# Kernel optimization log

Hardware: AMD Instinct MI355X
Metric: run time of the kernel (lower is better)

## Reference

```python
import jax, jax.numpy as jnp
import numpy as np

NEG_SLOPE = 0.2

def _gat_layer(x, src, dst, W, a_src, a_dst, bias, concat):
    # x: [N, F_in]; W: [F_in, H*C]; a_src/a_dst: [H, C]; bias: [H*C] or [C]
    N = x.shape[0]
    H, C = a_src.shape
    h = (x @ W).reshape(N, H, C)                      # node features per head
    e_src = jnp.einsum('nhc,hc->nh', h, a_src)        # [N, H]
    e_dst = jnp.einsum('nhc,hc->nh', h, a_dst)        # [N, H]
    e = jax.nn.leaky_relu(e_src[src] + e_dst[dst], NEG_SLOPE)  # [E, H]
    # segment softmax over incoming edges of each destination node
    m = jax.ops.segment_max(e, dst, num_segments=N)   # [N, H]
    p = jnp.exp(e - m[dst])
    denom = jax.ops.segment_sum(p, dst, num_segments=N)
    alpha = p / denom[dst]                            # [E, H]
    msg = h[src] * alpha[:, :, None]                  # [E, H, C]
    out = jax.ops.segment_sum(msg, dst, num_segments=N)  # [N, H, C]
    if concat:
        out = out.reshape(N, H * C) + bias
    else:
        out = out.mean(axis=1) + bias
    return out, alpha


def setup_inputs() -> dict:
    key = jax.random.key(0)
    ks = jax.random.split(key, 12)
    N, E = 20000, 320000
    F_in, Ch, Co, H = 256, 64, 64, 8
    x = jax.random.normal(ks[0], (N, F_in), dtype=jnp.float32)
    edge_index = jax.random.randint(ks[1], (2, E), 0, N, dtype=jnp.int64)
    s = 0.05
    return {
        'x': x,
        'edge_index': edge_index,
        'W1': jax.random.normal(ks[2], (F_in, H * Ch), dtype=jnp.float32) * s,
        'att_src1': jax.random.normal(ks[3], (H, Ch), dtype=jnp.float32) * s,
        'att_dst1': jax.random.normal(ks[4], (H, Ch), dtype=jnp.float32) * s,
        'b1': jnp.zeros((H * Ch,), dtype=jnp.float32),
        'W2': jax.random.normal(ks[5], (H * Ch, H * Co), dtype=jnp.float32) * s,
        'att_src2': jax.random.normal(ks[6], (H, Co), dtype=jnp.float32) * s,
        'att_dst2': jax.random.normal(ks[7], (H, Co), dtype=jnp.float32) * s,
        'b2': jnp.zeros((Co,), dtype=jnp.float32),
    }


def reference(x, edge_index, W1, att_src1, att_dst1, b1, W2, att_src2, att_dst2, b2):
    N = x.shape[0]
    # PyG GATConv adds self-loops by default
    loop = jnp.arange(N, dtype=edge_index.dtype)
    src = jnp.concatenate([edge_index[0], loop])
    dst = jnp.concatenate([edge_index[1], loop])
    h1, alpha1 = _gat_layer(x, src, dst, W1, att_src1, att_dst1, b1, concat=True)
    h1 = jax.nn.relu(h1)
    h2, alpha2 = _gat_layer(h1, src, dst, W2, att_src2, att_dst2, b2, concat=False)
    return h2, alpha1, alpha2
```

## Files before the change

### kernel.cpp

```cpp
#include <hip/hip_runtime.h>

#define H 8
#define C 64
#define HC 512
#define NEG 0.2f

typedef __attribute__((ext_vector_type(8))) _Float16 half8v;
typedef __attribute__((ext_vector_type(4))) _Float16 half4v;
typedef __attribute__((ext_vector_type(4))) float f32x4;

__device__ __forceinline__ float leaky(float x) { return x > 0.f ? x : NEG * x; }

#define GLOAD_LDS16(gp, lp) \
  __builtin_amdgcn_global_load_lds((const __attribute__((address_space(1))) unsigned int*)(gp), \
                                   (__attribute__((address_space(3))) unsigned int*)(lp), 16, 0, 0)

__global__ void k_degree(const int* __restrict__ ei, int E, int N, int* __restrict__ deg) {
    int e = blockIdx.x * blockDim.x + threadIdx.x;
    int Et = E + N;
    if (e >= Et) return;
    int d = (e < E) ? ei[E + e] : (e - E);
    atomicAdd(&deg[d], 1);
}

__global__ __launch_bounds__(1024) void k_scan(const int* __restrict__ deg, int N, int* __restrict__ row_start) {
    __shared__ int part[1024];
    int t = threadIdx.x;
    int chunk = (N + 1023) >> 10;
    int lo = t * chunk, hi = min(lo + chunk, N);
    int s = 0;
    for (int i = lo; i < hi; ++i) s += deg[i];
    part[t] = s;
    __syncthreads();
    for (int off = 1; off < 1024; off <<= 1) {
        int v = (t >= off) ? part[t - off] : 0;
        __syncthreads();
        part[t] += v;
        __syncthreads();
    }
    int base = (t == 0) ? 0 : part[t - 1];
    for (int i = lo; i < hi; ++i) { row_start[i] = base; base += deg[i]; }
    if (t == 1023) row_start[N] = part[1023];
}

__global__ void k_fill(const int* __restrict__ ei, int E, int N,
                       const int* __restrict__ row_start, int* __restrict__ cursor,
                       int* __restrict__ csr_src, int* __restrict__ csr_eid,
                       int* __restrict__ csr_dst) {
    int e = blockIdx.x * blockDim.x + threadIdx.x;
    int Et = E + N;
    if (e >= Et) return;
    int d, s;
    if (e < E) { s = ei[e]; d = ei[E + e]; } else { s = e - E; d = s; }
    int pos = atomicAdd(&cursor[d], 1);
    int idx = row_start[d] + pos;
    csr_src[idx] = s;
    csr_eid[idx] = e;
    csr_dst[idx] = d;
}

__global__ void k_tofp16(const float* __restrict__ in, _Float16* __restrict__ out, int n4) {
    int i = blockIdx.x * blockDim.x + threadIdx.x;
    if (i >= n4) return;
    float4 v = reinterpret_cast<const float4*>(in)[i];
    half4v h;
    h[0] = (_Float16)v.x; h[1] = (_Float16)v.y;
    h[2] = (_Float16)v.z; h[3] = (_Float16)v.w;
    reinterpret_cast<half4v*>(out)[i] = h;
}

__global__ void k_tcast(const float* __restrict__ W, _Float16* __restrict__ th, int K, int Nc) {
    int idx = blockIdx.x * blockDim.x + threadIdx.x;
    if (idx >= K * Nc) return;
    int c = idx / K, k = idx - c * K;
    th[idx] = (_Float16)W[(long)k * Nc + c];
}

__global__ __launch_bounds__(256) void k_gemm_mfma(const _Float16* __restrict__ A,
                                                   const _Float16* __restrict__ B,
                                                   _Float16* __restrict__ Cc, int M, int K, int Pb, int Mpad) {
    __shared__ _Float16 lA[8192], lB[8192];
    int bid = blockIdx.x;
    int panel = ((bid >> 5) << 3) + (bid & 7);
    int colb  = (bid >> 3) & 3;
    if (panel >= Pb) return;
    int tid = threadIdx.x;
    int w = tid >> 6, lane = tid & 63;
    int wr = w >> 1, wc = w & 1;
    int r0 = panel * 128, c0 = colb * 128;
    f32x4 acc[4][4] = {};
    int frag_off = ((lane >> 4) * 16 + (lane & 15)) * 8;

    int rb0 = tid >> 6, kc0 = (tid >> 4) & 3, r16_0 = tid & 15;
    int rb1 = (256 + tid) >> 6, kc1 = ((256 + tid) >> 4) & 3;
    long gaBase0 = (long)(r0 + rb0 * 16 + r16_0) * K + kc0 * 8;
    long gbBase0 = (long)(c0 + rb0 * 16 + r16_0) * K + kc0 * 8;
    long gaBase1 = (long)(r0 + rb1 * 16 + r16_0) * K + kc1 * 8;
    long gbBase1 = (long)(c0 + rb1 * 16 + r16_0) * K + kc1 * 8;
    int ldst0 = (w * 64) * 8;
    int ldst1 = (256 + w * 64) * 8;

#define STAGE(buf, k0)  do { \
        int off = (buf) * 4096; \
        GLOAD_LDS16(A + gaBase0 + (k0), lA + off + ldst0); \
        GLOAD_LDS16(B + gbBase0 + (k0), lB + off + ldst0); \
        GLOAD_LDS16(A + gaBase1 + (k0), lA + off + ldst1); \
        GLOAD_LDS16(B + gbBase1 + (k0), lB + off + ldst1); \
    } while (0)

    int nk = K >> 5;
    STAGE(0, 0);
    __syncthreads();
    int cur = 0;
    for (int t = 0; t < nk; ++t) {
        if (t + 1 < nk) STAGE(cur ^ 1, (t + 1) * 32);
        int off = cur * 4096;
        half8v fa[4], fb[4];
        #pragma unroll
        for (int m = 0; m < 4; ++m) {
            int sa = off + (wr * 4 + m) * 512 + frag_off;
            fa[m] = *reinterpret_cast<half8v*>(&lA[sa]);
            int sb = off + (wc * 4 + m) * 512 + frag_off;
            fb[m] = *reinterpret_cast<half8v*>(&lB[sb]);
        }
        #pragma unroll
        for (int m = 0; m < 4; ++m)
            #pragma unroll
            for (int n = 0; n < 4; ++n)
                acc[m][n] = __builtin_amdgcn_mfma_f32_16x16x32_f16(fa[m], fb[n], acc[m][n], 0, 0, 0);
        __syncthreads();
        cur ^= 1;
    }
#undef STAGE

    int head = colb * 2 + wc;
    long hbase = (long)head * Mpad * 64;
    #pragma unroll
    for (int m = 0; m < 4; ++m)
        #pragma unroll
        for (int j = 0; j < 4; ++j) {
            int gr = r0 + wr * 64 + m * 16 + (lane >> 4) * 4 + j;
            if (gr < M) {
                #pragma unroll
                for (int n = 0; n < 4; ++n)
                    Cc[hbase + (long)gr * 64 + n * 16 + (lane & 15)] = (_Float16)acc[m][n][j];
            }
        }
}

__global__ __launch_bounds__(512) void k_edot(const half8v* __restrict__ hp8,
                                              const float* __restrict__ a_src,
                                              const float* __restrict__ a_dst,
                                              float* __restrict__ e_src, float* __restrict__ e_dst,
                                              int N, int Mpad) {
    int h = threadIdx.x >> 6, lane = threadIdx.x & 63;
    int n8 = lane >> 3, cg = lane & 7;
    int n = blockIdx.x * 8 + n8;
    bool valid = (n < N);
    int nc = valid ? n : (N - 1);
    float as[8], ad[8];
    #pragma unroll
    for (int k = 0; k < 8; ++k) {
        as[k] = a_src[h * 64 + cg * 8 + k];
        ad[k] = a_dst[h * 64 + cg * 8 + k];
    }
    half8v hv = hp8[(long)h * Mpad * 8 + (long)nc * 8 + cg];
    float es = 0.f, ed = 0.f;
    #pragma unroll
    for (int k = 0; k < 8; ++k) {
        es = fmaf((float)hv[k], as[k], es);
        ed = fmaf((float)hv[k], ad[k], ed);
    }
    #pragma unroll
    for (int o = 1; o <= 4; o <<= 1) {
        es += __shfl_xor(es, o);
        ed += __shfl_xor(ed, o);
    }
    if (valid && cg == 0) {
        e_src[n * 8 + h] = es;
        e_dst[n * 8 + h] = ed;
    }
}

__global__ __launch_bounds__(512) void k_edge(const float* __restrict__ e_src,
                                              const float* __restrict__ e_dst,
                                              const int* __restrict__ row_start,
                                              const int* __restrict__ csr_src,
                                              int2* __restrict__ sp,
                                              float* __restrict__ inv_nm,
                                              float* __restrict__ inv_hm,
                                              int N, int Et) {
    int wid = threadIdx.x >> 6, lane = threadIdx.x & 63;
    int g = lane >> 5;
    int eg = (lane >> 3) & 3;
    int h = lane & 7;
    int n = blockIdx.x * 16 + wid * 2 + g;
    bool valid = (n < N);
    int nc = valid ? n : (N - 1);
    int row = row_start[nc];
    int deg = row_start[nc + 1] - row;
    float ed = e_dst[nc * 8 + h];
    long hEt = (long)h * Et;
    int it = (deg + 3) >> 2;
    int itmax = max(it, __shfl_xor(it, 32));
    const int* cs = csr_src + row + eg;
    int s_nf = cs[0];
    float psum = 0.f;
    for (int c = 0; c < itmax; ++c) {
        int s = s_nf;
        if (c + 1 < itmax) s_nf = cs[(c + 1) * 4];
        int e0 = c * 4 + eg;
        float es = e_src[s * 8 + h];
        float p = (e0 < deg) ? __expf(leaky(es + ed)) : 0.f;
        psum += p;
        if (valid && e0 < deg)
            sp[hEt + row + e0] = make_int2(s, __float_as_int(p));
    }
    psum += __shfl_xor(psum, 8);
    psum += __shfl_xor(psum, 16);
    float inv = 1.0f / psum;
    if (valid && eg == 0) {
        inv_nm[n * 8 + h] = inv;
        inv_hm[h * N + n] = inv;
    }
}

__global__ void k_alpha(const int* __restrict__ csr_dst, const int* __restrict__ csr_eid,
                        const int2* __restrict__ sp, const float* __restrict__ inv_nm,
                        float* __restrict__ alpha, int Et) {
    int idx = blockIdx.x * blockDim.x + threadIdx.x;
    if (idx >= Et) return;
    int d = csr_dst[idx], eid = csr_eid[idx];
    const float4* i4 = reinterpret_cast<const float4*>(inv_nm) + (long)d * 2;
    float4 i0 = i4[0], i1 = i4[1];
    float iv[8] = {i0.x, i0.y, i0.z, i0.w, i1.x, i1.y, i1.z, i1.w};
    float r[8];
    #pragma unroll
    for (int h = 0; h < 8; ++h)
        r[h] = __int_as_float(sp[(long)h * Et + idx].y) * iv[h];
    float4* o4 = reinterpret_cast<float4*>(alpha) + (long)eid * 2;
    o4[0] = make_float4(r[0], r[1], r[2], r[3]);
    o4[1] = make_float4(r[4], r[5], r[6], r[7]);
}

__global__ __launch_bounds__(256) void k_gather(const half8v* __restrict__ hp8,
                                                const int* __restrict__ row_start,
                                                const int2* __restrict__ sp,
                                                const float* __restrict__ inv_hm,
                                                const float* __restrict__ bias,
                                                _Float16* __restrict__ h1,
                                                _Float16* __restrict__ accq,
                                                int N, int Mpad, int Et, int concat) {
    int wid = threadIdx.x >> 6, lane = threadIdx.x & 63;
    int bid = blockIdx.x;
    int h = bid & 7;
    int g = lane >> 5;
    int eg = (lane >> 3) & 3;
    int cg = lane & 7;
    int n = (bid >> 3) * 8 + wid * 2 + g;
    bool valid = (n < N);
    int nc = valid ? n : (N - 1);
    const half8v* hpb = hp8 + (long)h * Mpad * 8 + cg;
    int row = row_start[nc];
    int deg = row_start[nc + 1] - row;
    int it = (deg + 15) >> 4;
    int itmax = max(it, __shfl_xor(it, 32));
    float acc[8] = {};
    const int2* pp = sp + (long)h * Et + row + eg * 4;
    int2 q0 = pp[0], q1 = pp[1], q2 = pp[2], q3 = pp[3];
    int ebase = eg * 4;
    for (int c = 0; c < itmax; ++c) {
        int2 a0 = q0, a1 = q1, a2 = q2, a3 = q3;
        if (c + 1 < itmax) {
            pp += 16;
            q0 = pp[0]; q1 = pp[1]; q2 = pp[2]; q3 = pp[3];
        }
        int e0 = c * 16 + ebase;
        float p0 = (e0 + 0 < deg) ? __int_as_float(a0.y) : 0.f;
        float p1 = (e0 + 1 < deg) ? __int_as_float(a1.y) : 0.f;
        float p2 = (e0 + 2 < deg) ? __int_as_float(a2.y) : 0.f;
        float p3 = (e0 + 3 < deg) ? __int_as_float(a3.y) : 0.f;
        half8v h0 = hpb[(long)a0.x * 8];
        half8v h1v = hpb[(long)a1.x * 8];
        half8v h2 = hpb[(long)a2.x * 8];
        half8v h3 = hpb[(long)a3.x * 8];
        #pragma unroll
        for (int k = 0; k < 8; ++k) {
            acc[k] = fmaf((float)h0[k], p0, acc[k]);
            acc[k] = fmaf((float)h1v[k], p1, acc[k]);
            acc[k] = fmaf((float)h2[k], p2, acc[k]);
            acc[k] = fmaf((float)h3[k], p3, acc[k]);
        }
    }
    #pragma unroll
    for (int o = 8; o <= 16; o <<= 1)
        #pragma unroll
        for (int k = 0; k < 8; ++k)
            acc[k] += __shfl_xor(acc[k], o);
    if (!valid) return;
    float inv = inv_hm[h * N + n];
    if (eg == 0) {
        if (concat) {
            half8v hh;
            #pragma unroll
            for (int k = 0; k < 8; ++k) {
                float v = fmaf(acc[k], inv, bias[h * 64 + cg * 8 + k]);
                v = v > 0.f ? v : 0.f;
                hh[k] = (_Float16)v;
            }
            reinterpret_cast<half8v*>(h1)[(long)n * 64 + h * 8 + cg] = hh;
        } else {
            half8v hv2;
            #pragma unroll
            for (int k = 0; k < 8; ++k) hv2[k] = (_Float16)(acc[k] * inv);
            reinterpret_cast<half8v*>(accq)[(long)h * Mpad * 8 + (long)n * 8 + cg] = hv2;
        }
    }
}

__global__ void k_mean(const _Float16* __restrict__ accq, const float* __restrict__ bias,
                       float* __restrict__ out, int N, int Mpad) {
    int i = blockIdx.x * blockDim.x + threadIdx.x;
    if (i >= N * 8) return;
    int n = i >> 3, cg = i & 7;
    float s[8] = {};
    #pragma unroll
    for (int h = 0; h < 8; ++h) {
        half8v v = reinterpret_cast<const half8v*>(accq)[(long)h * Mpad * 8 + (long)n * 8 + cg];
        #pragma unroll
        for (int k = 0; k < 8; ++k) s[k] += (float)v[k];
    }
    float4 r0, r1;
    r0.x = s[0] * 0.125f + bias[cg * 8 + 0];
    r0.y = s[1] * 0.125f + bias[cg * 8 + 1];
    r0.z = s[2] * 0.125f + bias[cg * 8 + 2];
    r0.w = s[3] * 0.125f + bias[cg * 8 + 3];
    r1.x = s[4] * 0.125f + bias[cg * 8 + 4];
    r1.y = s[5] * 0.125f + bias[cg * 8 + 5];
    r1.z = s[6] * 0.125f + bias[cg * 8 + 6];
    r1.w = s[7] * 0.125f + bias[cg * 8 + 7];
    float4* o4 = reinterpret_cast<float4*>(out + (long)n * 64 + cg * 8);
    o4[0] = r0;
    o4[1] = r1;
}

extern "C" void kernel_launch(void* const* d_in, const int* in_sizes, int n_in,
                              void* d_out, int out_size, void* d_ws, size_t ws_size,
                              hipStream_t stream) {
    const float* x   = (const float*)d_in[0];
    const int*   ei  = (const int*)d_in[1];
    const float* W1  = (const float*)d_in[2];
    const float* as1 = (const float*)d_in[3];
    const float* ad1 = (const float*)d_in[4];
    const float* b1  = (const float*)d_in[5];
    const float* W2  = (const float*)d_in[6];
    const float* as2 = (const float*)d_in[7];
    const float* ad2 = (const float*)d_in[8];
    const float* b2  = (const float*)d_in[9];

    int N  = in_sizes[0] / 256;
    int E  = in_sizes[1] / 2;
    int Et = E + N;
    int K1 = 256;
    int Mb   = (N + 127) / 128;
    int Mpad = Mb * 128;
    const int PAD = 64;

    float* out    = (float*)d_out;
    float* h2_out = out;
    float* alpha1 = out + (size_t)N * 64;
    float* alpha2 = alpha1 + (size_t)Et * H;

    _Float16* hpre = (_Float16*)d_ws;
    _Float16* h1   = hpre + (size_t)Mpad * HC;
    _Float16* accq = h1 + (size_t)Mpad * HC;
    _Float16* xh   = accq + (size_t)Mpad * HC;
    _Float16* W1t  = xh + (size_t)Mpad * K1;
    _Float16* W2t  = W1t + (size_t)HC * K1;
    float* eS     = (float*)(W2t + (size_t)HC * HC);
    float* eD     = eS + (size_t)N * H;
    float* invnm  = eD + (size_t)N * H;
    float* invhm  = invnm + (size_t)N * H;
    int2* sp      = (int2*)(invhm + (size_t)N * H);
    int*   deg    = (int*)(sp + (size_t)H * Et + PAD);
    int*   cursor = deg + N;
    int*   row_st = cursor + N;
    int*   csr_src= row_st + N + 1;
    int*   csr_eid= csr_src + Et + PAD;
    int*   csr_dst= csr_eid + Et;

    hipMemsetAsync(deg, 0, (size_t)2 * N * sizeof(int), stream);
    hipMemsetAsync(sp + (size_t)H * Et, 0, PAD * sizeof(int2), stream);
    hipMemsetAsync(csr_src + Et, 0, PAD * sizeof(int), stream);
    int tb = 256;
    k_degree<<<(Et + tb - 1) / tb, tb, 0, stream>>>(ei, E, N, deg);
    k_scan<<<1, 1024, 0, stream>>>(deg, N, row_st);
    k_fill<<<(Et + tb - 1) / tb, tb, 0, stream>>>(ei, E, N, row_st, cursor, csr_src, csr_eid, csr_dst);

    int n4 = N * K1 / 4;
    k_tofp16<<<(n4 + tb - 1) / tb, tb, 0, stream>>>(x, xh, n4);
    k_tcast<<<(K1 * HC + tb - 1) / tb, tb, 0, stream>>>(W1, W1t, K1, HC);
    k_tcast<<<(HC * HC + tb - 1) / tb, tb, 0, stream>>>(W2, W2t, HC, HC);

    int Pb8 = ((Mb + 7) / 8) * 8;
    int ggemm = Pb8 * 4;
    int gedot = (N + 7) / 8;
    int gedge = (N + 15) / 16;
    int ggath = ((N + 7) / 8) * 8;
    k_gemm_mfma<<<ggemm, 256, 0, stream>>>(xh, W1t, hpre, N, K1, Mb, Mpad);
    k_edot<<<gedot, 512, 0, stream>>>((const half8v*)hpre, as1, ad1, eS, eD, N, Mpad);
    k_edge<<<gedge, 512, 0, stream>>>(eS, eD, row_st, csr_src, sp, invnm, invhm, N, Et);
    k_alpha<<<(Et + tb - 1) / tb, tb, 0, stream>>>(csr_dst, csr_eid, sp, invnm, alpha1, Et);
    k_gather<<<ggath, 256, 0, stream>>>((const half8v*)hpre, row_st, sp, invhm,
                                        b1, h1, nullptr, N, Mpad, Et, 1);
    k_gemm_mfma<<<ggemm, 256, 0, stream>>>(h1, W2t, hpre, N, HC, Mb, Mpad);
    k_edot<<<gedot, 512, 0, stream>>>((const half8v*)hpre, as2, ad2, eS, eD, N, Mpad);
    k_edge<<<gedge, 512, 0, stream>>>(eS, eD, row_st, csr_src, sp, invnm, invhm, N, Et);
    k_alpha<<<(Et + tb - 1) / tb, tb, 0, stream>>>(csr_dst, csr_eid, sp, invnm, alpha2, Et);
    k_gather<<<ggath, 256, 0, stream>>>((const half8v*)hpre, row_st, sp, invhm,
                                        b2, nullptr, accq, N, Mpad, Et, 0);
    k_mean<<<(N * 8 + tb - 1) / tb, tb, 0, stream>>>(accq, b2, h2_out, N, Mpad);
}
```

Before: 281.9 us.

## Sort nodes by degree for balanced warps and fuse prep kernels

The scan kernel now builds a counting-sort permutation of nodes bucketed by in-degree, capped at 63. The edge and gather kernels process nodes in that order, so the two nodes sharing a wavefront have similar degree and less loop divergence. The fp16 casts of x, W1 and W2 are merged into one launch, and two memsets are merged into one. The cost is extra serial work in the single-block scan and scattered writes to the output and sp that lose node locality.

Measured after the change: 307.1 us. +8.9%, slower.

```diff
diff --git a/kernel.cpp b/kernel.cpp
--- a/kernel.cpp
+++ b/kernel.cpp
@@ -23,14 +23,18 @@
     atomicAdd(&deg[d], 1);
 }
 
-__global__ __launch_bounds__(1024) void k_scan(const int* __restrict__ deg, int N, int* __restrict__ row_start) {
+__global__ __launch_bounds__(1024) void k_scan(const int* __restrict__ deg, int N,
+                                               int* __restrict__ row_start,
+                                               int* __restrict__ perm) {
     __shared__ int part[1024];
+    __shared__ int bh[64], bo[64];
     int t = threadIdx.x;
     int chunk = (N + 1023) >> 10;
     int lo = t * chunk, hi = min(lo + chunk, N);
     int s = 0;
     for (int i = lo; i < hi; ++i) s += deg[i];
     part[t] = s;
+    if (t < 64) bh[t] = 0;
     __syncthreads();
     for (int off = 1; off < 1024; off <<= 1) {
         int v = (t >= off) ? part[t - off] : 0;
@@ -41,6 +45,18 @@
     int base = (t == 0) ? 0 : part[t - 1];
     for (int i = lo; i < hi; ++i) { row_start[i] = base; base += deg[i]; }
     if (t == 1023) row_start[N] = part[1023];
+    for (int i = lo; i < hi; ++i) atomicAdd(&bh[min(deg[i], 63)], 1);
+    __syncthreads();
+    if (t == 0) {
+        int run = 0;
+        for (int b = 0; b < 64; ++b) { bo[b] = run; run += bh[b]; }
+    }
+    __syncthreads();
+    for (int i = lo; i < hi; ++i) {
+        int b = min(deg[i], 63);
+        int pos = atomicAdd(&bo[b], 1);
+        perm[pos] = i;
+    }
 }
 
 __global__ void k_fill(const int* __restrict__ ei, int E, int N,
@@ -59,21 +75,29 @@
     csr_dst[idx] = d;
 }
 
-__global__ void k_tofp16(const float* __restrict__ in, _Float16* __restrict__ out, int n4) {
+__global__ void k_prep(const float* __restrict__ x, _Float16* __restrict__ xh, int n4,
+                       const float* __restrict__ W1, _Float16* __restrict__ W1t, int K1,
+                       const float* __restrict__ W2, _Float16* __restrict__ W2t) {
     int i = blockIdx.x * blockDim.x + threadIdx.x;
-    if (i >= n4) return;
-    float4 v = reinterpret_cast<const float4*>(in)[i];
-    half4v h;
-    h[0] = (_Float16)v.x; h[1] = (_Float16)v.y;
-    h[2] = (_Float16)v.z; h[3] = (_Float16)v.w;
-    reinterpret_cast<half4v*>(out)[i] = h;
-}
-
-__global__ void k_tcast(const float* __restrict__ W, _Float16* __restrict__ th, int K, int Nc) {
-    int idx = blockIdx.x * blockDim.x + threadIdx.x;
-    if (idx >= K * Nc) return;
-    int c = idx / K, k = idx - c * K;
-    th[idx] = (_Float16)W[(long)k * Nc + c];
+    if (i < n4) {
+        float4 v = reinterpret_cast<const float4*>(x)[i];
+        half4v h;
+        h[0] = (_Float16)v.x; h[1] = (_Float16)v.y;
+        h[2] = (_Float16)v.z; h[3] = (_Float16)v.w;
+        reinterpret_cast<half4v*>(xh)[i] = h;
+        return;
+    }
+    int j = i - n4;
+    if (j < K1 * HC) {
+        int c = j / K1, k = j - c * K1;
+        W1t[j] = (_Float16)W1[(long)k * HC + c];
+        return;
+    }
+    j -= K1 * HC;
+    if (j < HC * HC) {
+        int c = j / HC, k = j - c * HC;
+        W2t[j] = (_Float16)W2[(long)k * HC + c];
+    }
 }
 
 __global__ __launch_bounds__(256) void k_gemm_mfma(const _Float16* __restrict__ A,
@@ -186,6 +210,7 @@
                                               const float* __restrict__ e_dst,
                                               const int* __restrict__ row_start,
                                               const int* __restrict__ csr_src,
+                                              const int* __restrict__ perm,
                                               int2* __restrict__ sp,
                                               float* __restrict__ inv_nm,
                                               float* __restrict__ inv_hm,
@@ -194,12 +219,12 @@
     int g = lane >> 5;
     int eg = (lane >> 3) & 3;
     int h = lane & 7;
-    int n = blockIdx.x * 16 + wid * 2 + g;
-    bool valid = (n < N);
-    int nc = valid ? n : (N - 1);
-    int row = row_start[nc];
-    int deg = row_start[nc + 1] - row;
-    float ed = e_dst[nc * 8 + h];
+    int ni = blockIdx.x * 16 + wid * 2 + g;
+    bool valid = (ni < N);
+    int n = perm[valid ? ni : (N - 1)];
+    int row = row_start[n];
+    int deg = row_start[n + 1] - row;
+    float ed = e_dst[n * 8 + h];
     long hEt = (long)h * Et;
     int it = (deg + 3) >> 2;
     int itmax = max(it, __shfl_xor(it, 32));
@@ -247,6 +272,7 @@
                                                 const int* __restrict__ row_start,
                                                 const int2* __restrict__ sp,
                                                 const float* __restrict__ inv_hm,
+                                                const int* __restrict__ perm,
                                                 const float* __restrict__ bias,
                                                 _Float16* __restrict__ h1,
                                                 _Float16* __restrict__ accq,
@@ -257,12 +283,12 @@
     int g = lane >> 5;
     int eg = (lane >> 3) & 3;
     int cg = lane & 7;
-    int n = (bid >> 3) * 8 + wid * 2 + g;
-    bool valid = (n < N);
-    int nc = valid ? n : (N - 1);
+    int ni = (bid >> 3) * 8 + wid * 2 + g;
+    bool valid = (ni < N);
+    int n = perm[valid ? ni : (N - 1)];
     const half8v* hpb = hp8 + (long)h * Mpad * 8 + cg;
-    int row = row_start[nc];
-    int deg = row_start[nc + 1] - row;
+    int row = row_start[n];
+    int deg = row_start[n + 1] - row;
     int it = (deg + 15) >> 4;
     int itmax = max(it, __shfl_xor(it, 32));
     float acc[8] = {};
@@ -385,22 +411,21 @@
     int*   deg    = (int*)(sp + (size_t)H * Et + PAD);
     int*   cursor = deg + N;
     int*   row_st = cursor + N;
-    int*   csr_src= row_st + N + 1;
+    int*   perm   = row_st + N + 1;
+    int*   csr_src= perm + N;
     int*   csr_eid= csr_src + Et + PAD;
     int*   csr_dst= csr_eid + Et;
 
-    hipMemsetAsync(deg, 0, (size_t)2 * N * sizeof(int), stream);
-    hipMemsetAsync(sp + (size_t)H * Et, 0, PAD * sizeof(int2), stream);
+    hipMemsetAsync(sp + (size_t)H * Et, 0, PAD * sizeof(int2) + (size_t)2 * N * sizeof(int), stream);
     hipMemsetAsync(csr_src + Et, 0, PAD * sizeof(int), stream);
     int tb = 256;
     k_degree<<<(Et + tb - 1) / tb, tb, 0, stream>>>(ei, E, N, deg);
-    k_scan<<<1, 1024, 0, stream>>>(deg, N, row_st);
+    k_scan<<<1, 1024, 0, stream>>>(deg, N, row_st, perm);
     k_fill<<<(Et + tb - 1) / tb, tb, 0, stream>>>(ei, E, N, row_st, cursor, csr_src, csr_eid, csr_dst);
 
     int n4 = N * K1 / 4;
-    k_tofp16<<<(n4 + tb - 1) / tb, tb, 0, stream>>>(x, xh, n4);
-    k_tcast<<<(K1 * HC + tb - 1) / tb, tb, 0, stream>>>(W1, W1t, K1, HC);
-    k_tcast<<<(HC * HC + tb - 1) / tb, tb, 0, stream>>>(W2, W2t, HC, HC);
+    int prep_total = n4 + K1 * HC + HC * HC;
+    k_prep<<<(prep_total + tb - 1) / tb, tb, 0, stream>>>(x, xh, n4, W1, W1t, K1, W2, W2t);
 
     int Pb8 = ((Mb + 7) / 8) * 8;
     int ggemm = Pb8 * 4;
@@ -409,15 +434,15 @@
     int ggath = ((N + 7) / 8) * 8;
     k_gemm_mfma<<<ggemm, 256, 0, stream>>>(xh, W1t, hpre, N, K1, Mb, Mpad);
     k_edot<<<gedot, 512, 0, stream>>>((const half8v*)hpre, as1, ad1, eS, eD, N, Mpad);
-    k_edge<<<gedge, 512, 0, stream>>>(eS, eD, row_st, csr_src, sp, invnm, invhm, N, Et);
+    k_edge<<<gedge, 512, 0, stream>>>(eS, eD, row_st, csr_src, perm, sp, invnm, invhm, N, Et);
     k_alpha<<<(Et + tb - 1) / tb, tb, 0, stream>>>(csr_dst, csr_eid, sp, invnm, alpha1, Et);
-    k_gather<<<ggath, 256, 0, stream>>>((const half8v*)hpre, row_st, sp, invhm,
+    k_gather<<<ggath, 256, 0, stream>>>((const half8v*)hpre, row_st, sp, invhm, perm,
                                         b1, h1, nullptr, N, Mpad, Et, 1);
     k_gemm_mfma<<<ggemm, 256, 0, stream>>>(h1, W2t, hpre, N, HC, Mb, Mpad);
     k_edot<<<gedot, 512, 0, stream>>>((const half8v*)hpre, as2, ad2, eS, eD, N, Mpad);
-    k_edge<<<gedge, 512, 0, stream>>>(eS, eD, row_st, csr_src, sp, invnm, invhm, N, Et);
+    k_edge<<<gedge, 512, 0, stream>>>(eS, eD, row_st, csr_src, perm, sp, invnm, invhm, N, Et);
     k_alpha<<<(Et + tb - 1) / tb, tb, 0, stream>>>(csr_dst, csr_eid, sp, invnm, alpha2, Et);
-    k_gather<<<ggath, 256, 0, stream>>>((const half8v*)hpre, row_st, sp, invhm,
+    k_gather<<<ggath, 256, 0, stream>>>((const half8v*)hpre, row_st, sp, invhm, perm,
                                         b2, nullptr, accq, N, Mpad, Et, 0);
     k_mean<<<(N * 8 + tb - 1) / tb, tb, 0, stream>>>(accq, b2, h2_out, N, Mpad);
 }
```
